# Optimization experiments

Measured on AMD Instinct MI355X. Metric: run time of the kernel, lower is better.

Reference implementation:

```python
import jax, jax.numpy as jnp
import numpy as np
import math

B, C, TC, H, W = 8, 256, 512, 48, 48
EPS = 1e-6

def setup_inputs() -> dict:
    key = jax.random.key(0)
    kx, kt, kq, kk, kv = jax.random.split(key, 5)
    x = jax.random.normal(kx, (B, C, H, W), dtype=jnp.float32)
    token = jax.random.normal(kt, (B, TC, H, W), dtype=jnp.float32)
    # xavier_uniform for 1x1 conv weights [out, in]
    def xavier(k, fan_out, fan_in):
        a = math.sqrt(6.0 / (fan_in + fan_out))
        return jax.random.uniform(k, (fan_out, fan_in), dtype=jnp.float32, minval=-a, maxval=a)
    Wq = xavier(kq, C, C)
    Wk = xavier(kk, C, TC)
    Wv = xavier(kv, C, TC)
    alpha = jnp.float32(0.5)  # nonzero so the attention path affects the output
    return {"x": x, "token": token, "Wq": Wq, "Wk": Wk, "Wv": Wv, "alpha": alpha}

def reference(x, token, Wq, Wk, Wv, alpha):
    # 1x1 convs == per-pixel GEMMs over the channel dim
    q = jnp.einsum('oc,bchw->bohw', Wq, x)       # [B,C,H,W]
    k = jnp.einsum('oc,bchw->bohw', Wk, token)   # [B,C,H,W]
    v = jnp.einsum('oc,bchw->bohw', Wv, token)   # [B,C,H,W]
    b, c, h, w = q.shape
    n = h * w
    qf = q.reshape(b, c, n).transpose(0, 2, 1)   # [B,N,C]
    kf = k.reshape(b, c, n)                      # [B,C,N]
    vf = v.reshape(b, c, n).transpose(0, 2, 1)   # [B,N,C]
    # cosine normalization over the channel dim (F.normalize with eps clamp)
    qn = qf / jnp.maximum(jnp.linalg.norm(qf, axis=-1, keepdims=True), EPS)
    kn = kf / jnp.maximum(jnp.linalg.norm(kf, axis=1, keepdims=True), EPS)
    attn = jnp.einsum('bnc,bcm->bnm', qn, kn) / math.sqrt(c)  # [B,N,N]
    attn = jax.nn.softmax(attn, axis=-1)
    out = jnp.einsum('bnm,bmc->bnc', attn, vf)   # [B,N,C]
    out = out.transpose(0, 2, 1).reshape(b, c, h, w)
    return x + alpha * out
```

## Files before the change

### kernel.cpp

```cpp
#include <hip/hip_runtime.h>

#define B_   8
#define C_   256
#define TC_  512
#define HW_  2304
#define EPS_ 1e-6f

typedef __bf16 bf16_t;
typedef __bf16 bf16x8 __attribute__((ext_vector_type(8)));
typedef __bf16 bf16x4_t __attribute__((ext_vector_type(4)));
typedef float  f32x4 __attribute__((ext_vector_type(4)));
typedef unsigned int  u32;
typedef unsigned int  u32x2 __attribute__((ext_vector_type(2)));
typedef unsigned int  u32x4 __attribute__((ext_vector_type(4)));
typedef long long     i64;
typedef unsigned char u8;

__device__ __forceinline__ void g2l16(const void* g, void* l) {
    __builtin_amdgcn_global_load_lds(
        (const __attribute__((address_space(1))) unsigned int*)g,
        (__attribute__((address_space(3))) unsigned int*)l, 16, 0, 0);
}

__device__ __forceinline__ u8 to_fp8(float v) {
    return (u8)(__builtin_amdgcn_cvt_pk_fp8_f32(v, v, 0, false) & 0xff);
}

__global__ __launch_bounds__(256)
void wfrag_kernel(const float* __restrict__ wq, const float* __restrict__ wk,
                  const float* __restrict__ wv,
                  bf16_t* __restrict__ oq, bf16_t* __restrict__ ok,
                  bf16_t* __restrict__ ov)
{
    const int fid = blockIdx.x * 4 + (threadIdx.x >> 6);
    const int lane = threadIdx.x & 63;
    const int l16 = lane & 15, quad = lane >> 4;

    const float* src; bf16_t* dst; int cin, f;
    if (fid < 128)      { src = wq; dst = oq; cin = C_;  f = fid; }
    else if (fid < 384) { src = wk; dst = ok; cin = TC_; f = fid - 128; }
    else                { src = wv; dst = ov; cin = TC_; f = fid - 384; }
    const int nks = cin / 32;
    const int ot = f / nks, ks = f % nks;

    const float* s = src + (size_t)(ot * 16 + l16) * cin + ks * 32 + quad * 8;
    float4 a = *(const float4*)(s);
    float4 b = *(const float4*)(s + 4);
    bf16x8 o;
    o[0] = (__bf16)a.x; o[1] = (__bf16)a.y; o[2] = (__bf16)a.z; o[3] = (__bf16)a.w;
    o[4] = (__bf16)b.x; o[5] = (__bf16)b.y; o[6] = (__bf16)b.z; o[7] = (__bf16)b.w;
    *(bf16x8*)(dst + (size_t)f * 512 + lane * 8) = o;
}

template<int CIN, bool DO_V>
__global__ __launch_bounds__(256, 4)
void convqkv_kernel(const float* __restrict__ X, const bf16_t* __restrict__ Wa,
                    const bf16_t* __restrict__ Wvp, u8* __restrict__ outA,
                    u8* __restrict__ outV)
{
    const int bid = blockIdx.x;
    const int b  = bid & 7;
    const int n0 = (bid >> 3) * 16;
    const int tid = threadIdx.x;
    const int wv = tid >> 6;
    const int lane = tid & 63;
    const int quad = lane >> 4, l16 = lane & 15;
    const int NKS = CIN / 32;

    __shared__ bf16_t T[16][CIN + 8];
    __shared__ float ssp[4][16];

    {
        const float* Xb = X + (size_t)b * CIN * HW_ + n0;
        const int cl = tid >> 2;
        const int n4 = (tid & 3) * 4;
#pragma unroll
        for (int cp = 0; cp < CIN; cp += 64) {
            float4 v = *(const float4*)(Xb + (size_t)(cp + cl) * HW_ + n4);
            T[n4 + 0][cp + cl] = (__bf16)v.x;
            T[n4 + 1][cp + cl] = (__bf16)v.y;
            T[n4 + 2][cp + cl] = (__bf16)v.z;
            T[n4 + 3][cp + cl] = (__bf16)v.w;
        }
    }
    __syncthreads();

    bf16x8 af[CIN / 32];
#pragma unroll
    for (int ks = 0; ks < CIN / 32; ks++)
        af[ks] = *(const bf16x8*)(&T[l16][ks * 32 + quad * 8]);

    const int ot0 = wv * 4;

    f32x4 accK[4];
#pragma unroll
    for (int p = 0; p < 4; p++) accK[p] = (f32x4){0.f, 0.f, 0.f, 0.f};
    {
        const bf16_t* wbase = Wa + ((size_t)ot0 * NKS) * 512 + lane * 8;
#pragma unroll
        for (int ks = 0; ks < CIN / 32; ks++)
#pragma unroll
            for (int p = 0; p < 4; p++) {
                bf16x8 bw = *(const bf16x8*)(wbase + (size_t)(p * NKS + ks) * 512);
                accK[p] = __builtin_amdgcn_mfma_f32_16x16x32_bf16(af[ks], bw, accK[p], 0, 0, 0);
            }
    }

    {
        float ssr[4];
#pragma unroll
        for (int r = 0; r < 4; r++) {
            float ss = accK[0][r] * accK[0][r] + accK[1][r] * accK[1][r]
                     + accK[2][r] * accK[2][r] + accK[3][r] * accK[3][r];
            ss += __shfl_xor(ss, 1);
            ss += __shfl_xor(ss, 2);
            ss += __shfl_xor(ss, 4);
            ss += __shfl_xor(ss, 8);
            ssr[r] = ss;
        }
        if (l16 == 0) {
#pragma unroll
            for (int r = 0; r < 4; r++) ssp[wv][quad * 4 + r] = ssr[r];
        }
    }

    f32x4 accV[4];
    if (DO_V) {
#pragma unroll
        for (int p = 0; p < 4; p++) accV[p] = (f32x4){0.f, 0.f, 0.f, 0.f};
        const bf16_t* wbase = Wvp + ((size_t)ot0 * NKS) * 512 + lane * 8;
#pragma unroll
        for (int ks = 0; ks < CIN / 32; ks++)
#pragma unroll
            for (int p = 0; p < 4; p++) {
                bf16x8 aw = *(const bf16x8*)(wbase + (size_t)(p * NKS + ks) * 512);
                accV[p] = __builtin_amdgcn_mfma_f32_16x16x32_bf16(aw, af[ks], accV[p], 0, 0, 0);
            }
    }

    __syncthreads();

    float scale[4];
#pragma unroll
    for (int r = 0; r < 4; r++) {
        int px = quad * 4 + r;
        float s = ssp[0][px] + ssp[1][px] + ssp[2][px] + ssp[3][px];
        scale[r] = 1.0f / fmaxf(sqrtf(s), EPS_);
    }
    {
        u8* oa = outA + ((size_t)b * HW_ + n0 + quad * 4) * C_ + l16;
#pragma unroll
        for (int p = 0; p < 4; p++)
#pragma unroll
            for (int r = 0; r < 4; r++)
                oa[(size_t)r * C_ + (ot0 + p) * 16] = to_fp8(accK[p][r] * scale[r]);
    }

    if (DO_V) {
#pragma unroll
        for (int p = 0; p < 4; p++)
#pragma unroll
            for (int r = 0; r < 4; r++)
                outV[((size_t)b * C_ + (ot0 + p) * 16 + quad * 4 + r) * HW_ + n0 + l16]
                    = to_fp8(accV[p][r]);
    }
}

__global__ __launch_bounds__(256, 2)
void attn_part_kernel(const u8* __restrict__ q8, const u8* __restrict__ k8,
                      const u8* __restrict__ v8,
                      bf16_t* __restrict__ Opart, float* __restrict__ lpart,
                      int tilesPerSplit, int JS)
{
    const int bid = blockIdx.x;
    const int b   = bid & 7;
    const int rr  = bid >> 3;
    const int js  = rr % JS;
    const int mt  = rr / JS;
    const int wv   = threadIdx.x >> 6;
    const int lane = threadIdx.x & 63;
    const int quad = lane >> 4;
    const int l16  = lane & 15;
    const int row0 = mt * 128 + wv * 32;
    const int jbase = js * tilesPerSplit * 32;

    const u8* qb = q8 + (size_t)b * HW_ * C_;
    const u8* kb = k8 + (size_t)b * HW_ * C_;
    const u8* vb = v8 + (size_t)b * C_ * HW_;

    __shared__ u8 Kbuf[2][8192];
    __shared__ u8 Vbuf[2][8192];
    __shared__ u8 Pt[4][1536];

    i64 aq0[8], aq1[8];
    {
        const u8* r0 = qb + (size_t)(row0 + l16) * C_ + quad * 8;
        const u8* r1 = r0 + 16 * C_;
#pragma unroll
        for (int t = 0; t < 8; t++) {
            aq0[t] = *(const i64*)(r0 + t * 32);
            aq1[t] = *(const i64*)(r1 + t * 32);
        }
    }

    f32x4 O0[16], O1[16];
#pragma unroll
    for (int i = 0; i < 16; i++) {
        O0[i] = (f32x4){0.f, 0.f, 0.f, 0.f};
        O1[i] = (f32x4){0.f, 0.f, 0.f, 0.f};
    }
    float lsum0[4] = {0.f, 0.f, 0.f, 0.f};
    float lsum1[4] = {0.f, 0.f, 0.f, 0.f};

    const int kj = lane & 31;
    const int kh = lane >> 5;
    const int vg = lane & 1;
    const int vc = lane >> 1;

#define STAGE(bufi, j0g)                                                       \
    {                                                                          \
        _Pragma("unroll")                                                      \
        for (int p = 0; p < 2; p++) {                                          \
            int i = wv * 2 + p;                                                \
            int s = i * 2 + kh;                                                \
            g2l16(kb + (size_t)((j0g) + kj) * C_ + s * 16,                     \
                  &Kbuf[bufi][i * 1024]);                                      \
        }                                                                      \
        _Pragma("unroll")                                                      \
        for (int p = 0; p < 2; p++) {                                          \
            int i = wv * 2 + p;                                                \
            int c = i * 32 + vc;                                               \
            g2l16(vb + (size_t)c * HW_ + (j0g) + vg * 16,                      \
                  &Vbuf[bufi][i * 1024]);                                      \
        }                                                                      \
    }

    STAGE(0, jbase)

    u8* pw = &Pt[wv][0];
    const int koff = (quad >> 1) * 512 + l16 * 16 + (quad & 1) * 8;
    const u32 sel = (quad < 2) ? 0x06040200u : 0x07050301u;

    for (int tt = 0; tt < tilesPerSplit; tt++) {
        __syncthreads();
        if (tt + 1 < tilesPerSplit) STAGE((tt + 1) & 1, jbase + (tt + 1) * 32)

        const u8* Kb = Kbuf[tt & 1];
        const u8* Vb = Vbuf[tt & 1];

        f32x4 s00 = (f32x4){0.f,0.f,0.f,0.f}, s01 = (f32x4){0.f,0.f,0.f,0.f};
        f32x4 s10 = (f32x4){0.f,0.f,0.f,0.f}, s11 = (f32x4){0.f,0.f,0.f,0.f};
#pragma unroll
        for (int t = 0; t < 8; t++) {
            i64 bk0 = *(const i64*)(Kb + t * 1024 + koff);
            i64 bk1 = *(const i64*)(Kb + t * 1024 + koff + 256);
            s00 = __builtin_amdgcn_mfma_f32_16x16x32_fp8_fp8(aq0[t], bk0, s00, 0, 0, 0);
            s01 = __builtin_amdgcn_mfma_f32_16x16x32_fp8_fp8(aq0[t], bk1, s01, 0, 0, 0);
            s10 = __builtin_amdgcn_mfma_f32_16x16x32_fp8_fp8(aq1[t], bk0, s10, 0, 0, 0);
            s11 = __builtin_amdgcn_mfma_f32_16x16x32_fp8_fp8(aq1[t], bk1, s11, 0, 0, 0);
        }
#pragma unroll
        for (int r = 0; r < 4; r++) {
            float p00 = __expf(s00[r] * 0.0625f), p01 = __expf(s01[r] * 0.0625f);
            float p10 = __expf(s10[r] * 0.0625f), p11 = __expf(s11[r] * 0.0625f);
            lsum0[r] += p00 + p01;
            lsum1[r] += p10 + p11;
            u32 w0 = __builtin_amdgcn_cvt_pk_fp8_f32(p00, p01, 0, false);
            u32 w1 = __builtin_amdgcn_cvt_pk_fp8_f32(p10, p11, 0, false);
            int ro = (quad * 4 + r) * 48 + l16 * 2;
            *(short*)(pw + ro)       = (short)w0;
            *(short*)(pw + 768 + ro) = (short)w1;
        }
        i64 ap0, ap1;
        {
            u32x4 d = *(const u32x4*)(pw + l16 * 48 + (quad & 1) * 16);
            u32 lo = __builtin_amdgcn_perm(d[1], d[0], sel);
            u32 hi = __builtin_amdgcn_perm(d[3], d[2], sel);
            ap0 = ((i64)hi << 32) | (i64)lo;
            u32x4 e = *(const u32x4*)(pw + 768 + l16 * 48 + (quad & 1) * 16);
            lo = __builtin_amdgcn_perm(e[1], e[0], sel);
            hi = __builtin_amdgcn_perm(e[3], e[2], sel);
            ap1 = ((i64)hi << 32) | (i64)lo;
        }
#pragma unroll
        for (int ct = 0; ct < 16; ct++) {
            i64 bv = *(const i64*)(Vb + ct * 512 + l16 * 32 + quad * 8);
            O0[ct] = __builtin_amdgcn_mfma_f32_16x16x32_fp8_fp8(ap0, bv, O0[ct], 0, 0, 0);
            O1[ct] = __builtin_amdgcn_mfma_f32_16x16x32_fp8_fp8(ap1, bv, O1[ct], 0, 0, 0);
        }
    }

#pragma unroll
    for (int r = 0; r < 4; r++) {
        float t0 = lsum0[r], t1 = lsum1[r];
        t0 += __shfl_xor(t0, 1); t0 += __shfl_xor(t0, 2);
        t0 += __shfl_xor(t0, 4); t0 += __shfl_xor(t0, 8);
        t1 += __shfl_xor(t1, 1); t1 += __shfl_xor(t1, 2);
        t1 += __shfl_xor(t1, 4); t1 += __shfl_xor(t1, 8);
        lsum0[r] = t0; lsum1[r] = t1;
    }
    float* lp = lpart + (size_t)(js * B_ + b) * HW_;
    if (l16 == 0) {
        float4 a0; a0.x = lsum0[0]; a0.y = lsum0[1]; a0.z = lsum0[2]; a0.w = lsum0[3];
        float4 a1; a1.x = lsum1[0]; a1.y = lsum1[1]; a1.z = lsum1[2]; a1.w = lsum1[3];
        *(float4*)(lp + row0 + quad * 4)      = a0;
        *(float4*)(lp + row0 + 16 + quad * 4) = a1;
    }
    bf16_t* op = Opart + (size_t)(js * B_ + b) * C_ * HW_;
#pragma unroll
    for (int ct = 0; ct < 16; ct++) {
        int c = ct * 16 + l16;
        bf16x4_t v0, v1;
        v0[0] = (__bf16)O0[ct][0]; v0[1] = (__bf16)O0[ct][1];
        v0[2] = (__bf16)O0[ct][2]; v0[3] = (__bf16)O0[ct][3];
        v1[0] = (__bf16)O1[ct][0]; v1[1] = (__bf16)O1[ct][1];
        v1[2] = (__bf16)O1[ct][2]; v1[3] = (__bf16)O1[ct][3];
        *(bf16x4_t*)(op + (size_t)c * HW_ + row0 + quad * 4)      = v0;
        *(bf16x4_t*)(op + (size_t)c * HW_ + row0 + 16 + quad * 4) = v1;
    }
#undef STAGE
}

__global__ __launch_bounds__(256)
void epilogue_kernel(const float* __restrict__ x, const bf16_t* __restrict__ Opart,
                     const float* __restrict__ lpart, const float* __restrict__ alphaPtr,
                     float* __restrict__ out, int JS)
{
    const float a = *alphaPtr;
    const size_t S = (size_t)B_ * C_ * HW_;
    size_t flat = ((size_t)blockIdx.x * 256 + threadIdx.x) * 4;
    int bc = (int)(flat / HW_);
    int n  = (int)(flat % HW_);
    int b  = bc >> 8;
    float4 xv = *(const float4*)(x + flat);
    float s0 = 0.f, s1 = 0.f, s2 = 0.f, s3 = 0.f;
    float l0 = 0.f, l1 = 0.f, l2 = 0.f, l3 = 0.f;
    for (int js = 0; js < JS; js++) {
        bf16x4_t ov = *(const bf16x4_t*)(Opart + (size_t)js * S + flat);
        s0 += (float)ov[0]; s1 += (float)ov[1];
        s2 += (float)ov[2]; s3 += (float)ov[3];
        float4 lv = *(const float4*)(lpart + (size_t)(js * B_ + b) * HW_ + n);
        l0 += lv.x; l1 += lv.y; l2 += lv.z; l3 += lv.w;
    }
    float4 r;
    r.x = xv.x + a * s0 / l0;
    r.y = xv.y + a * s1 / l1;
    r.z = xv.z + a * s2 / l2;
    r.w = xv.w + a * s3 / l3;
    *(float4*)(out + flat) = r;
}

extern "C" void kernel_launch(void* const* d_in, const int* in_sizes, int n_in,
                              void* d_out, int out_size, void* d_ws, size_t ws_size,
                              hipStream_t stream)
{
    (void)in_sizes; (void)n_in; (void)out_size;
    const float* x     = (const float*)d_in[0];
    const float* token = (const float*)d_in[1];
    const float* Wq    = (const float*)d_in[2];
    const float* Wk    = (const float*)d_in[3];
    const float* Wv    = (const float*)d_in[4];
    const float* alpha = (const float*)d_in[5];
    float* out = (float*)d_out;

    const size_t S = (size_t)B_ * HW_ * C_;

    int JS = 8;
    for (;;) {
        size_t need = (12 + 2 * (size_t)JS) * S
                    + (size_t)JS * B_ * HW_ * 4 + (size_t)B_ * HW_ * 4;
        if (need <= ws_size || JS == 1) break;
        JS >>= 1;
    }
    const int tilesPerSplit = (HW_ / 32) / JS;

    char* ws = (char*)d_ws;
    bf16_t* WqL   = (bf16_t*)(ws + 6 * S);
    bf16_t* WkL   = WqL + (size_t)C_ * C_;
    bf16_t* WvL   = WkL + (size_t)C_ * TC_;
    u8*     q8    = (u8*)(ws + 7 * S);
    u8*     k8    = (u8*)(ws + 8 * S);
    u8*     v8    = (u8*)(ws + 9 * S);
    bf16_t* Opart = (bf16_t*)(ws + 12 * S);
    float*  lpart = (float*)(ws + (12 + 2 * (size_t)JS) * S);

    wfrag_kernel<<<dim3(160), dim3(256), 0, stream>>>(Wq, Wk, Wv, WqL, WkL, WvL);
    convqkv_kernel<C_,  false><<<dim3(B_ * HW_ / 16), dim3(256), 0, stream>>>(x,     WqL, nullptr, q8, nullptr);
    convqkv_kernel<TC_, true ><<<dim3(B_ * HW_ / 16), dim3(256), 0, stream>>>(token, WkL, WvL,     k8, v8);
    attn_part_kernel<<<dim3(JS * B_ * (HW_ / 128)), dim3(256), 0, stream>>>(q8, k8, v8, Opart, lpart, tilesPerSplit, JS);
    epilogue_kernel<<<dim3((int)(S / 1024)), dim3(256), 0, stream>>>(x, Opart, lpart, alpha, out, JS);
}
```

Baseline: 243.2 us.

## Halve attention query tile per wave to raise occupancy and swizzle V LDS layout

```diff
diff --git a/kernel.cpp b/kernel.cpp
--- a/kernel.cpp
+++ b/kernel.cpp
@@ -166,7 +166,7 @@
     }
 }
 
-__global__ __launch_bounds__(256, 2)
+__global__ __launch_bounds__(256, 4)
 void attn_part_kernel(const u8* __restrict__ q8, const u8* __restrict__ k8,
                       const u8* __restrict__ v8,
                       bf16_t* __restrict__ Opart, float* __restrict__ lpart,
@@ -181,7 +181,7 @@
     const int lane = threadIdx.x & 63;
     const int quad = lane >> 4;
     const int l16  = lane & 15;
-    const int row0 = mt * 128 + wv * 32;
+    const int row0 = mt * 64 + wv * 16;
     const int jbase = js * tilesPerSplit * 32;
 
     const u8* qb = q8 + (size_t)b * HW_ * C_;
@@ -190,31 +190,23 @@
 
     __shared__ u8 Kbuf[2][8192];
     __shared__ u8 Vbuf[2][8192];
-    __shared__ u8 Pt[4][1536];
-
-    i64 aq0[8], aq1[8];
+    __shared__ u8 Pt[4][896];
+
+    i64 aq[8];
     {
         const u8* r0 = qb + (size_t)(row0 + l16) * C_ + quad * 8;
-        const u8* r1 = r0 + 16 * C_;
-#pragma unroll
-        for (int t = 0; t < 8; t++) {
-            aq0[t] = *(const i64*)(r0 + t * 32);
-            aq1[t] = *(const i64*)(r1 + t * 32);
-        }
-    }
-
-    f32x4 O0[16], O1[16];
-#pragma unroll
-    for (int i = 0; i < 16; i++) {
-        O0[i] = (f32x4){0.f, 0.f, 0.f, 0.f};
-        O1[i] = (f32x4){0.f, 0.f, 0.f, 0.f};
-    }
-    float lsum0[4] = {0.f, 0.f, 0.f, 0.f};
-    float lsum1[4] = {0.f, 0.f, 0.f, 0.f};
+#pragma unroll
+        for (int t = 0; t < 8; t++) aq[t] = *(const i64*)(r0 + t * 32);
+    }
+
+    f32x4 O[16];
+#pragma unroll
+    for (int i = 0; i < 16; i++) O[i] = (f32x4){0.f, 0.f, 0.f, 0.f};
+    float lsum[4] = {0.f, 0.f, 0.f, 0.f};
 
     const int kj = lane & 31;
     const int kh = lane >> 5;
-    const int vg = lane & 1;
+    const int vg = (lane & 1) ^ ((lane >> 3) & 1);
     const int vc = lane >> 1;
 
 #define STAGE(bufi, j0g)                                                       \
@@ -238,7 +230,9 @@
     STAGE(0, jbase)
 
     u8* pw = &Pt[wv][0];
-    const int koff = (quad >> 1) * 512 + l16 * 16 + (quad & 1) * 8;
+    const int koff  = (quad >> 1) * 512 + l16 * 16 + (quad & 1) * 8;
+    const int vbase = l16 * 32 + ((((quad >> 1) ^ (l16 >> 2)) & 1) << 4)
+                    + (quad & 1) * 8;
     const u32 sel = (quad < 2) ? 0x06040200u : 0x07050301u;
 
     for (int tt = 0; tt < tilesPerSplit; tt++) {
@@ -249,74 +243,56 @@
         const u8* Vb = Vbuf[tt & 1];
 
         f32x4 s00 = (f32x4){0.f,0.f,0.f,0.f}, s01 = (f32x4){0.f,0.f,0.f,0.f};
-        f32x4 s10 = (f32x4){0.f,0.f,0.f,0.f}, s11 = (f32x4){0.f,0.f,0.f,0.f};
 #pragma unroll
         for (int t = 0; t < 8; t++) {
             i64 bk0 = *(const i64*)(Kb + t * 1024 + koff);
             i64 bk1 = *(const i64*)(Kb + t * 1024 + koff + 256);
-            s00 = __builtin_amdgcn_mfma_f32_16x16x32_fp8_fp8(aq0[t], bk0, s00, 0, 0, 0);
-            s01 = __builtin_amdgcn_mfma_f32_16x16x32_fp8_fp8(aq0[t], bk1, s01, 0, 0, 0);
-            s10 = __builtin_amdgcn_mfma_f32_16x16x32_fp8_fp8(aq1[t], bk0, s10, 0, 0, 0);
-            s11 = __builtin_amdgcn_mfma_f32_16x16x32_fp8_fp8(aq1[t], bk1, s11, 0, 0, 0);
+            s00 = __builtin_amdgcn_mfma_f32_16x16x32_fp8_fp8(aq[t], bk0, s00, 0, 0, 0);
+            s01 = __builtin_amdgcn_mfma_f32_16x16x32_fp8_fp8(aq[t], bk1, s01, 0, 0, 0);
         }
 #pragma unroll
         for (int r = 0; r < 4; r++) {
             float p00 = __expf(s00[r] * 0.0625f), p01 = __expf(s01[r] * 0.0625f);
-            float p10 = __expf(s10[r] * 0.0625f), p11 = __expf(s11[r] * 0.0625f);
-            lsum0[r] += p00 + p01;
-            lsum1[r] += p10 + p11;
+            lsum[r] += p00 + p01;
             u32 w0 = __builtin_amdgcn_cvt_pk_fp8_f32(p00, p01, 0, false);
-            u32 w1 = __builtin_amdgcn_cvt_pk_fp8_f32(p10, p11, 0, false);
-            int ro = (quad * 4 + r) * 48 + l16 * 2;
-            *(short*)(pw + ro)       = (short)w0;
-            *(short*)(pw + 768 + ro) = (short)w1;
-        }
-        i64 ap0, ap1;
+            *(short*)(pw + (quad * 4 + r) * 56 + l16 * 2) = (short)w0;
+        }
+        i64 ap0;
         {
-            u32x4 d = *(const u32x4*)(pw + l16 * 48 + (quad & 1) * 16);
-            u32 lo = __builtin_amdgcn_perm(d[1], d[0], sel);
-            u32 hi = __builtin_amdgcn_perm(d[3], d[2], sel);
+            const u8* pr = pw + l16 * 56 + (quad & 1) * 16;
+            u32x2 dA = *(const u32x2*)(pr);
+            u32x2 dB = *(const u32x2*)(pr + 8);
+            u32 lo = __builtin_amdgcn_perm(dA[1], dA[0], sel);
+            u32 hi = __builtin_amdgcn_perm(dB[1], dB[0], sel);
             ap0 = ((i64)hi << 32) | (i64)lo;
-            u32x4 e = *(const u32x4*)(pw + 768 + l16 * 48 + (quad & 1) * 16);
-            lo = __builtin_amdgcn_perm(e[1], e[0], sel);
-            hi = __builtin_amdgcn_perm(e[3], e[2], sel);
-            ap1 = ((i64)hi << 32) | (i64)lo;
         }
 #pragma unroll
         for (int ct = 0; ct < 16; ct++) {
-            i64 bv = *(const i64*)(Vb + ct * 512 + l16 * 32 + quad * 8);
-            O0[ct] = __builtin_amdgcn_mfma_f32_16x16x32_fp8_fp8(ap0, bv, O0[ct], 0, 0, 0);
-            O1[ct] = __builtin_amdgcn_mfma_f32_16x16x32_fp8_fp8(ap1, bv, O1[ct], 0, 0, 0);
+            i64 bv = *(const i64*)(Vb + ct * 512 + vbase);
+            O[ct] = __builtin_amdgcn_mfma_f32_16x16x32_fp8_fp8(ap0, bv, O[ct], 0, 0, 0);
         }
     }
 
 #pragma unroll
     for (int r = 0; r < 4; r++) {
-        float t0 = lsum0[r], t1 = lsum1[r];
+        float t0 = lsum[r];
         t0 += __shfl_xor(t0, 1); t0 += __shfl_xor(t0, 2);
         t0 += __shfl_xor(t0, 4); t0 += __shfl_xor(t0, 8);
-        t1 += __shfl_xor(t1, 1); t1 += __shfl_xor(t1, 2);
-        t1 += __shfl_xor(t1, 4); t1 += __shfl_xor(t1, 8);
-        lsum0[r] = t0; lsum1[r] = t1;
+        lsum[r] = t0;
     }
     float* lp = lpart + (size_t)(js * B_ + b) * HW_;
     if (l16 == 0) {
-        float4 a0; a0.x = lsum0[0]; a0.y = lsum0[1]; a0.z = lsum0[2]; a0.w = lsum0[3];
-        float4 a1; a1.x = lsum1[0]; a1.y = lsum1[1]; a1.z = lsum1[2]; a1.w = lsum1[3];
-        *(float4*)(lp + row0 + quad * 4)      = a0;
-        *(float4*)(lp + row0 + 16 + quad * 4) = a1;
+        float4 a0; a0.x = lsum[0]; a0.y = lsum[1]; a0.z = lsum[2]; a0.w = lsum[3];
+        *(float4*)(lp + row0 + quad * 4) = a0;
     }
     bf16_t* op = Opart + (size_t)(js * B_ + b) * C_ * HW_;
 #pragma unroll
     for (int ct = 0; ct < 16; ct++) {
         int c = ct * 16 + l16;
-        bf16x4_t v0, v1;
-        v0[0] = (__bf16)O0[ct][0]; v0[1] = (__bf16)O0[ct][1];
-        v0[2] = (__bf16)O0[ct][2]; v0[3] = (__bf16)O0[ct][3];
-        v1[0] = (__bf16)O1[ct][0]; v1[1] = (__bf16)O1[ct][1];
-        v1[2] = (__bf16)O1[ct][2]; v1[3] = (__bf16)O1[ct][3];
-        *(bf16x4_t*)(op + (size_t)c * HW_ + row0 + quad * 4)      = v0;
-        *(bf16x4_t*)(op + (size_t)c * HW_ + row0 + 16 + quad * 4) = v1;
+        bf16x4_t v0;
+        v0[0] = (__bf16)O[ct][0]; v0[1] = (__bf16)O[ct][1];
+        v0[2] = (__bf16)O[ct][2]; v0[3] = (__bf16)O[ct][3];
+        *(bf16x4_t*)(op + (size_t)c * HW_ + row0 + quad * 4) = v0;
     }
 #undef STAGE
 }
@@ -387,6 +363,6 @@
     wfrag_kernel<<<dim3(160), dim3(256), 0, stream>>>(Wq, Wk, Wv, WqL, WkL, WvL);
     convqkv_kernel<C_,  false><<<dim3(B_ * HW_ / 16), dim3(256), 0, stream>>>(x,     WqL, nullptr, q8, nullptr);
     convqkv_kernel<TC_, true ><<<dim3(B_ * HW_ / 16), dim3(256), 0, stream>>>(token, WkL, WvL,     k8, v8);
-    attn_part_kernel<<<dim3(JS * B_ * (HW_ / 128)), dim3(256), 0, stream>>>(q8, k8, v8, Opart, lpart, tilesPerSplit, JS);
+    attn_part_kernel<<<dim3(JS * B_ * (HW_ / 64)), dim3(256), 0, stream>>>(q8, k8, v8, Opart, lpart, tilesPerSplit, JS);
     epilogue_kernel<<<dim3((int)(S / 1024)), dim3(256), 0, stream>>>(x, Opart, lpart, alpha, out, JS);
 }
```

Measured after the change: 236.7 us. 1.03x faster.
